# Performance work log

Hardware: AMD Instinct MI355X
Metric: run time of the kernel (lower is better)

## Reference

```python
import jax, jax.numpy as jnp
import numpy as np

NEG_SLOPE = 0.2

def gat_layer(x, src, dst, W, a_src, a_dst, bias, heads, out_ch, concat):
    N = x.shape[0]
    h = (x @ W).reshape(N, heads, out_ch)                      # [N,H,C]
    alpha_s = jnp.sum(h * a_src, axis=-1)                      # [N,H]
    alpha_d = jnp.sum(h * a_dst, axis=-1)                      # [N,H]
    e = jax.nn.leaky_relu(alpha_s[src] + alpha_d[dst], NEG_SLOPE)  # [E,H]
    m = jax.ops.segment_max(e, dst, num_segments=N)            # segment softmax over incoming edges
    e = jnp.exp(e - m[dst])
    denom = jax.ops.segment_sum(e, dst, num_segments=N)
    alpha = e / denom[dst]                                     # [E,H]
    out = jax.ops.segment_sum(alpha[:, :, None] * h[src], dst, num_segments=N)  # [N,H,C]
    out = out.reshape(N, heads * out_ch) if concat else out.mean(axis=1)
    return out + bias

def _glorot(key, shape, fan):
    return jax.random.normal(key, shape, dtype=jnp.float32) * (1.0 / np.sqrt(fan))

def setup_inputs() -> dict:
    key = jax.random.key(0)
    ks = jax.random.split(key, 16)
    N, E, F_IN, H = 50000, 1600000, 128, 2
    x = jax.random.normal(ks[0], (N, F_IN), dtype=jnp.float32)
    edge_index = jax.random.randint(ks[1], (2, E), 0, N, dtype=jnp.int32)
    w1  = _glorot(ks[2], (F_IN, H * 32), F_IN)
    as1 = _glorot(ks[3], (H, 32), 32); ad1 = _glorot(ks[4], (H, 32), 32)
    b1  = jnp.zeros((H * 32,), jnp.float32)
    w2  = _glorot(ks[5], (H * 32, H * 64), H * 32)
    as2 = _glorot(ks[6], (H, 64), 64); ad2 = _glorot(ks[7], (H, 64), 64)
    b2  = jnp.zeros((H * 64,), jnp.float32)
    # layer 3: 128 -> 64, heads=1, concat=False
    w3  = _glorot(ks[8], (H * 64, 64), H * 64)
    as3 = _glorot(ks[9], (1, 64), 64); ad3 = _glorot(ks[10], (1, 64), 64)
    b3  = jnp.zeros((64,), jnp.float32)
    fcw = _glorot(ks[11], (64, 512), 64)
    fcb = jnp.zeros((512,), jnp.float32)
    return dict(x=x, edge_index=edge_index, w1=w1, as1=as1, ad1=ad1, b1=b1,
                w2=w2, as2=as2, ad2=ad2, b2=b2, w3=w3, as3=as3, ad3=ad3, b3=b3,
                fcw=fcw, fcb=fcb)

def reference(x, edge_index, w1, as1, ad1, b1, w2, as2, ad2, b2, w3, as3, ad3, b3, fcw, fcb):
    N = x.shape[0]
    # PyG GATConv default: add self-loops
    loops = jnp.arange(N, dtype=edge_index.dtype)
    src = jnp.concatenate([edge_index[0], loops])
    dst = jnp.concatenate([edge_index[1], loops])
    h = jax.nn.relu(gat_layer(x, src, dst, w1, as1, ad1, b1, heads=2, out_ch=32, concat=True))
    h = jax.nn.relu(gat_layer(h, src, dst, w2, as2, ad2, b2, heads=2, out_ch=64, concat=True))
    h = jax.nn.relu(gat_layer(h, src, dst, w3, as3, ad3, b3, heads=1, out_ch=64, concat=False))
    return jax.nn.relu(h @ fcw + fcb)
```

## Files before the change

kernel.cpp:

```cpp
#include <hip/hip_runtime.h>
#include <hip/hip_fp16.h>
#include <math.h>


typedef _Float16 h2_t __attribute__((ext_vector_type(2)));
typedef _Float16 f16x8 __attribute__((ext_vector_type(8)));
typedef float f32x4 __attribute__((ext_vector_type(4)));

__device__ __forceinline__ h2_t as_h2(unsigned int u) {
    union { unsigned int u; h2_t h; } x; x.u = u; return x.h;
}

__device__ __forceinline__ float fdot2(h2_t a, h2_t b, float c) {
#if __has_builtin(__builtin_amdgcn_fdot2)
    return __builtin_amdgcn_fdot2(a, b, c, false);
#else
    return c + (float)a[0] * (float)b[0] + (float)a[1] * (float)b[1];
#endif
}

__global__ void cvt_kernel(
        const float* __restrict__ x, __half* __restrict__ xh, int n4,
        const float* __restrict__ w1, const float* __restrict__ w2,
        const float* __restrict__ w3, const float* __restrict__ fcw,
        __half* __restrict__ o1, __half* __restrict__ o2,
        __half* __restrict__ o3, __half* __restrict__ o4T,
        int XB) {
    const int b = blockIdx.x;
    if (b < XB) {
        int i = b * 256 + threadIdx.x;
        if (i < n4) {
            float4 v = ((const float4*)x)[i];
            __half2 a, c;
            a.x = (__half)v.x; a.y = (__half)v.y;
            c.x = (__half)v.z; c.y = (__half)v.w;
            ((__half2*)xh)[2 * i]     = a;
            ((__half2*)xh)[2 * i + 1] = c;
        }
    } else {
        int i = (b - XB) * 256 + threadIdx.x;
        if (i < 8192)       o1[i]         = (__half)w1[i];
        else if (i < 16384) o2[i - 8192]  = (__half)w2[i - 8192];
        else if (i < 24576) o3[i - 16384] = (__half)w3[i - 16384];
        else if (i < 57344) {
            int j = i - 24576;
            int k = j >> 9, c = j & 511;
            o4T[c * 64 + k] = (__half)fcw[j];
        }
    }
}

#define SCAN_NB 256

__global__ __launch_bounds__(256) void scanA_kernel(const int* __restrict__ cnt,
                                                    int N, int* __restrict__ bsum) {
    __shared__ int red[256];
    const int chunk = (N + SCAN_NB - 1) / SCAN_NB;
    const int lo = blockIdx.x * chunk;
    const int len = min(N - lo, chunk);
    int s = 0;
    for (int i = threadIdx.x; i < len; i += 256) s += cnt[lo + i];
    red[threadIdx.x] = s;
    __syncthreads();
    for (int off = 128; off >= 1; off >>= 1) {
        if (threadIdx.x < off) red[threadIdx.x] += red[threadIdx.x + off];
        __syncthreads();
    }
    if (threadIdx.x == 0) bsum[blockIdx.x] = red[0];
}

__global__ __launch_bounds__(256) void scanB_kernel(int* __restrict__ bsum,
                                                    int* __restrict__ bbase) {
    __shared__ int s[256];
    int v = bsum[threadIdx.x];
    s[threadIdx.x] = v;
    __syncthreads();
    for (int off = 1; off < 256; off <<= 1) {
        int t = (threadIdx.x >= off) ? s[threadIdx.x - off] : 0;
        __syncthreads();
        s[threadIdx.x] += t;
        __syncthreads();
    }
    bbase[threadIdx.x] = s[threadIdx.x] - v;
}

__global__ __launch_bounds__(256) void scanC_kernel(const int* __restrict__ cnt,
                                                    int N, int Etot,
                                                    const int* __restrict__ bbase,
                                                    int* __restrict__ row_ptr) {
    __shared__ int s[256];
    const int chunk = (N + SCAN_NB - 1) / SCAN_NB;
    const int lo = blockIdx.x * chunk;
    const int len = min(N - lo, chunk);
    const int t = threadIdx.x;
    int v = (t < len) ? cnt[lo + t] : 0;
    s[t] = v;
    __syncthreads();
    for (int off = 1; off < 256; off <<= 1) {
        int u = (t >= off) ? s[t - off] : 0;
        __syncthreads();
        s[t] += u;
        __syncthreads();
    }
    if (t < len) row_ptr[lo + t] = bbase[blockIdx.x] + s[t] - v;
    if (blockIdx.x == 0 && t == 0) row_ptr[N] = Etot;
}

__global__ void scatter_kernel(const int* __restrict__ ei, int E, int N,
                               const int* __restrict__ row_ptr,
                               const int* __restrict__ rank,
                               int* __restrict__ csr_src) {
    const int Etot = E + N;
    const int T = gridDim.x * blockDim.x;
    int e = blockIdx.x * blockDim.x + threadIdx.x;
#pragma unroll 4
    for (int u = 0; u < 4; ++u, e += T) {
        if (e < Etot) {
            int src, dst;
            if (e < E) { src = ei[e]; dst = ei[E + e]; }
            else       { src = e - E; dst = e - E; }
            csr_src[row_ptr[dst] + rank[e]] = src;
        }
    }
}

template <int K, int CHUNK, int RB, int ALPHA, bool COUNT>
__global__ __launch_bounds__(256) void gemm16_kernel(
        const __half* __restrict__ in,
        const __half* __restrict__ Wh,
        __half* __restrict__ out,
        const float* __restrict__ a_src,
        const float* __restrict__ a_dst,
        float* __restrict__ alpS,
        float* __restrict__ alpD,
        int N, int M,
        const int* __restrict__ ei, int E,
        int* __restrict__ cnt, int* __restrict__ rank,
        int GGEMM) {
    constexpr int PL = CHUNK / 64;
    constexpr int K4 = K / 4;
    __shared__ uint2 wlds[K4 * CHUNK];

    if (COUNT && blockIdx.x >= GGEMM) {
        const int Etot = E + N;
        const int T = (gridDim.x - GGEMM) * 256;
        int e = (blockIdx.x - GGEMM) * 256 + threadIdx.x;
#pragma unroll 7
        for (int u = 0; u < 7; ++u, e += T) {
            if (e < Etot) {
                int dst = (e < E) ? ei[E + e] : (e - E);
                rank[e] = atomicAdd(&cnt[dst], 1);
            }
        }
        return;
    }
    const int GSTRIDE = COUNT ? GGEMM : gridDim.x;

    const unsigned short* wsrc = (const unsigned short*)Wh;
    for (int idx = threadIdx.x; idx < K4 * CHUNK; idx += 256) {
        int k4 = idx / CHUNK, c = idx % CHUNK;
        const unsigned short* wp = wsrc + (size_t)(4 * k4) * M + c;
        uint2 v;
        v.x = (unsigned int)wp[0]     | ((unsigned int)wp[M] << 16);
        v.y = (unsigned int)wp[2 * M] | ((unsigned int)wp[3 * M] << 16);
        wlds[idx] = v;
    }
    __syncthreads();

    const int wid  = threadIdx.x >> 6;
    const int lane = threadIdx.x & 63;

    float aSv[PL], aDv[PL];
#pragma unroll
    for (int j = 0; j < PL; ++j) {
        aSv[j] = a_src[lane + 64 * j];
        aDv[j] = a_dst[lane + 64 * j];
    }

    const int groups = (N + RB - 1) / RB;
    for (int g = blockIdx.x * 4 + wid; g < groups; g += GSTRIDE * 4) {
        const int n0 = g * RB;
        const bool full = (n0 + RB <= N);

        float acc[RB][PL];
#pragma unroll
        for (int r = 0; r < RB; ++r)
#pragma unroll
            for (int j = 0; j < PL; ++j) acc[r][j] = 0.0f;

        const uint2* xp = (const uint2*)(in + (size_t)n0 * K);

        if (full) {
            uint2 xv[RB], xn[RB];
#pragma unroll
            for (int r = 0; r < RB; ++r) xv[r] = xp[r * K4];
#pragma unroll 2
            for (int k4 = 0; k4 < K4; ++k4) {
                if (k4 + 1 < K4) {
#pragma unroll
                    for (int r = 0; r < RB; ++r)
                        xn[r] = xp[r * K4 + k4 + 1];
                }
#pragma unroll
                for (int j = 0; j < PL; ++j) {
                    uint2 wv = wlds[k4 * CHUNK + lane + 64 * j];
#pragma unroll
                    for (int r = 0; r < RB; ++r) {
                        acc[r][j] = fdot2(as_h2(xv[r].x), as_h2(wv.x), acc[r][j]);
                        acc[r][j] = fdot2(as_h2(xv[r].y), as_h2(wv.y), acc[r][j]);
                    }
                }
                if (k4 + 1 < K4) {
#pragma unroll
                    for (int r = 0; r < RB; ++r) xv[r] = xn[r];
                }
            }
        } else {
#pragma unroll 1
            for (int k4 = 0; k4 < K4; ++k4) {
#pragma unroll 1
                for (int r = 0; r < RB; ++r) {
                    if (n0 + r >= N) break;
                    uint2 xr = xp[(size_t)r * K4 + k4];
#pragma unroll
                    for (int j = 0; j < PL; ++j) {
                        uint2 wv = wlds[k4 * CHUNK + lane + 64 * j];
                        acc[r][j] = fdot2(as_h2(xr.x), as_h2(wv.x), acc[r][j]);
                        acc[r][j] = fdot2(as_h2(xr.y), as_h2(wv.y), acc[r][j]);
                    }
                }
            }
        }

#pragma unroll
        for (int r = 0; r < RB; ++r) {
            if (!full && n0 + r >= N) break;
            const int n = n0 + r;
#pragma unroll
            for (int j = 0; j < PL; ++j)
                out[(size_t)n * M + lane + 64 * j] = (__half)acc[r][j];

            float ps[PL], pd[PL];
#pragma unroll
            for (int j = 0; j < PL; ++j) { ps[j] = acc[r][j] * aSv[j]; pd[j] = acc[r][j] * aDv[j]; }
            const int m0 = (ALPHA == 1) ? 16 : 32;
            for (int mm = m0; mm >= 1; mm >>= 1) {
#pragma unroll
                for (int j = 0; j < PL; ++j) {
                    ps[j] += __shfl_xor(ps[j], mm, 64);
                    pd[j] += __shfl_xor(pd[j], mm, 64);
                }
            }
            if (ALPHA == 1) {
                if ((lane & 31) == 0) {
                    int idx = n * 2 + (lane >> 5);
                    alpS[idx] = ps[0]; alpD[idx] = pd[0];
                }
            } else if (ALPHA == 2) {
                if (lane == 0) {
#pragma unroll
                    for (int j = 0; j < PL; ++j) {
                        alpS[n * 2 + j] = ps[j]; alpD[n * 2 + j] = pd[j];
                    }
                }
            } else {
                if (lane == 0) { alpS[n] = ps[0]; alpD[n] = pd[0]; }
            }
        }
    }
}

__global__ __launch_bounds__(256) void fcmfma_kernel(
        const __half* __restrict__ in,
        const __half* __restrict__ WT,
        const float* __restrict__ bias,
        float* __restrict__ out,
        int N, int NT) {
    const int wid  = threadIdx.x >> 6;
    const int lane = threadIdx.x & 63;
    const int cb = blockIdx.y * 256 + wid * 64;
    const int r  = lane & 15;
    const int kg = lane >> 4;

    f16x8 bfrag[4][2];
#pragma unroll
    for (int t = 0; t < 4; ++t)
#pragma unroll
        for (int kf = 0; kf < 2; ++kf)
            bfrag[t][kf] = *(const f16x8*)(WT + (size_t)(cb + t * 16 + r) * 64 + kf * 32 + kg * 8);
    float bs[4];
#pragma unroll
    for (int t = 0; t < 4; ++t) bs[t] = bias[cb + t * 16 + r];

    const int rt0 = blockIdx.x * 5;
#pragma unroll 1
    for (int q = 0; q < 5; ++q) {
        const int rt = rt0 + q;
        if (rt >= NT) break;
        const int n0 = rt * 16;
        f16x8 a0 = *(const f16x8*)(in + (size_t)(n0 + r) * 64 + kg * 8);
        f16x8 a1 = *(const f16x8*)(in + (size_t)(n0 + r) * 64 + 32 + kg * 8);
#pragma unroll
        for (int t = 0; t < 4; ++t) {
            f32x4 acc = {0.0f, 0.0f, 0.0f, 0.0f};
            acc = __builtin_amdgcn_mfma_f32_16x16x32_f16(a0, bfrag[t][0], acc, 0, 0, 0);
            acc = __builtin_amdgcn_mfma_f32_16x16x32_f16(a1, bfrag[t][1], acc, 0, 0, 0);
#pragma unroll
            for (int i = 0; i < 4; ++i) {
                int grow = n0 + kg * 4 + i;
                if (grow < N)
                    out[(size_t)grow * 512 + cb + t * 16 + r] = fmaxf(acc[i] + bs[t], 0.0f);
            }
        }
    }
}

template <int H, int C>
__global__ __launch_bounds__(256) void aggregate_kernel(
        const __half* __restrict__ h,
        const float* __restrict__ alpha_s,
        const float* __restrict__ alpha_d,
        const int* __restrict__ row_ptr,
        const int* __restrict__ csr_src,
        const float* __restrict__ bias,
        __half* __restrict__ out, int N) {
    constexpr int M = H * C;
    __shared__ int   ss[4][64];
    __shared__ float sp[4][128];
    const int wid  = threadIdx.x >> 6;
    const int lane = threadIdx.x & 63;
    const int n = blockIdx.x * 4 + wid;
    if (n >= N) return;

    const int lo = row_ptr[n], hi = row_ptr[n + 1];
    const int myhead = (H == 2) ? (lane / C) : 0;

    float adv[H];
#pragma unroll
    for (int t = 0; t < H; ++t) adv[t] = alpha_d[n * H + t];

    float m[H], den[H], acc = 0.0f;
#pragma unroll
    for (int t = 0; t < H; ++t) { m[t] = -INFINITY; den[t] = 0.0f; }

    for (int e0 = lo; e0 < hi; e0 += 64) {
        const int idx = e0 + lane;
        const bool valid = idx < hi;
        const int src_l = csr_src[valid ? idx : hi - 1];

        float lg[H];
        if (H == 2) {
            float2 as = ((const float2*)alpha_s)[src_l];
            lg[0] = as.x + adv[0];
            lg[1] = as.y + adv[1];
        } else {
            lg[0] = alpha_s[src_l] + adv[0];
        }
#pragma unroll
        for (int t = 0; t < H; ++t) {
            float v = lg[t];
            v = v > 0.0f ? v : 0.2f * v;
            lg[t] = valid ? v : -INFINITY;
        }
        float cm[H];
#pragma unroll
        for (int t = 0; t < H; ++t) cm[t] = lg[t];
        for (int mm = 32; mm >= 1; mm >>= 1) {
#pragma unroll
            for (int t = 0; t < H; ++t)
                cm[t] = fmaxf(cm[t], __shfl_xor(cm[t], mm, 64));
        }
        float sc[H];
#pragma unroll
        for (int t = 0; t < H; ++t) {
            float mnew = fmaxf(m[t], cm[t]);
            sc[t] = __expf(m[t] - mnew);
            den[t] *= sc[t];
            m[t] = mnew;
        }
        acc *= (H == 1) ? sc[0] : (myhead == 0 ? sc[0] : sc[1]);

        float p[H], dsum[H];
#pragma unroll
        for (int t = 0; t < H; ++t) { p[t] = __expf(lg[t] - m[t]); dsum[t] = p[t]; }
        for (int mm = 32; mm >= 1; mm >>= 1) {
#pragma unroll
            for (int t = 0; t < H; ++t)
                dsum[t] += __shfl_xor(dsum[t], mm, 64);
        }
#pragma unroll
        for (int t = 0; t < H; ++t) den[t] += dsum[t];

        ss[wid][lane] = src_l;
        if (H == 2) ((float2*)sp[wid])[lane] = make_float2(p[0], p[1]);
        else        sp[wid][lane] = p[0];

        int nu = hi - e0; if (nu > 64) nu = 64;
        int u = 0;
#pragma unroll 1
        for (; u + 8 <= nu; u += 8) {
            int su[8];
#pragma unroll
            for (int t = 0; t < 8; ++t)
                su[t] = __builtin_amdgcn_readfirstlane(ss[wid][u + t]);
            float hv[8];
#pragma unroll
            for (int t = 0; t < 8; ++t)
                hv[t] = __half2float(h[(size_t)su[t] * M + lane]);
            if (H == 2) {
                const float2* pb = (const float2*)sp[wid];
#pragma unroll
                for (int t = 0; t < 8; ++t) {
                    float2 q = pb[u + t];
                    acc += (myhead == 0 ? q.x : q.y) * hv[t];
                }
            } else {
#pragma unroll
                for (int t = 0; t < 8; ++t)
                    acc += sp[wid][u + t] * hv[t];
            }
        }
#pragma unroll 1
        for (; u < nu; ++u) {
            int su = __builtin_amdgcn_readfirstlane(ss[wid][u]);
            float hv = __half2float(h[(size_t)su * M + lane]);
            if (H == 2) {
                float2 q = ((const float2*)sp[wid])[u];
                acc += (myhead == 0 ? q.x : q.y) * hv;
            } else {
                acc += sp[wid][u] * hv;
            }
        }
    }

    float dv = (H == 1) ? den[0] : (myhead == 0 ? den[0] : den[1]);
    float v = acc / dv + bias[lane];
    out[(size_t)n * M + lane] = (__half)fmaxf(v, 0.0f);
}

__global__ __launch_bounds__(256) void aggregate2_kernel(
        const __half* __restrict__ h,
        const float* __restrict__ alpha_s,
        const float* __restrict__ alpha_d,
        const int* __restrict__ row_ptr,
        const int* __restrict__ csr_src,
        const float* __restrict__ bias,
        __half* __restrict__ out, int N) {
    __shared__ int   ss[4][64];
    __shared__ float sp[4][64];
    const int wid  = threadIdx.x >> 6;
    const int lane = threadIdx.x & 63;
    const int gw   = blockIdx.x * 4 + wid;
    const int n    = gw >> 1;
    const int hd   = gw & 1;
    if (n >= N) return;

    const int lo = row_ptr[n], hi = row_ptr[n + 1];
    const float adv = alpha_d[n * 2 + hd];

    float m = -INFINITY, den = 0.0f, acc = 0.0f;

    for (int e0 = lo; e0 < hi; e0 += 64) {
        const int idx = e0 + lane;
        const bool valid = idx < hi;
        const int src_l = csr_src[valid ? idx : hi - 1];

        float lg = alpha_s[src_l * 2 + hd] + adv;
        lg = lg > 0.0f ? lg : 0.2f * lg;
        if (!valid) lg = -INFINITY;

        float cm = lg;
        for (int mm = 32; mm >= 1; mm >>= 1)
            cm = fmaxf(cm, __shfl_xor(cm, mm, 64));

        float mnew = fmaxf(m, cm);
        float sc = __expf(m - mnew);
        den *= sc; acc *= sc; m = mnew;

        float p = __expf(lg - m), ds = p;
        for (int mm = 32; mm >= 1; mm >>= 1)
            ds += __shfl_xor(ds, mm, 64);
        den += ds;

        ss[wid][lane] = src_l;
        sp[wid][lane] = p;

        int nu = hi - e0; if (nu > 64) nu = 64;
        int u = 0;
#pragma unroll 1
        for (; u + 8 <= nu; u += 8) {
            int su[8];
#pragma unroll
            for (int t = 0; t < 8; ++t)
                su[t] = __builtin_amdgcn_readfirstlane(ss[wid][u + t]);
            float hv[8];
#pragma unroll
            for (int t = 0; t < 8; ++t)
                hv[t] = __half2float(h[(size_t)su[t] * 128 + hd * 64 + lane]);
#pragma unroll
            for (int t = 0; t < 8; ++t)
                acc += sp[wid][u + t] * hv[t];
        }
#pragma unroll 1
        for (; u < nu; ++u) {
            int su = __builtin_amdgcn_readfirstlane(ss[wid][u]);
            acc += sp[wid][u] * __half2float(h[(size_t)su * 128 + hd * 64 + lane]);
        }
    }

    float v = acc / den + bias[hd * 64 + lane];
    out[(size_t)n * 128 + hd * 64 + lane] = (__half)fmaxf(v, 0.0f);
}


extern "C" void kernel_launch(void* const* d_in, const int* in_sizes, int n_in,
                              void* d_out, int out_size, void* d_ws, size_t ws_size,
                              hipStream_t stream) {
    const float* x   = (const float*)d_in[0];
    const int*   ei  = (const int*)  d_in[1];
    const float* w1  = (const float*)d_in[2];
    const float* as1 = (const float*)d_in[3];
    const float* ad1 = (const float*)d_in[4];
    const float* b1  = (const float*)d_in[5];
    const float* w2  = (const float*)d_in[6];
    const float* as2 = (const float*)d_in[7];
    const float* ad2 = (const float*)d_in[8];
    const float* b2  = (const float*)d_in[9];
    const float* w3  = (const float*)d_in[10];
    const float* as3 = (const float*)d_in[11];
    const float* ad3 = (const float*)d_in[12];
    const float* b3  = (const float*)d_in[13];
    const float* fcw = (const float*)d_in[14];
    const float* fcb = (const float*)d_in[15];
    float* out = (float*)d_out;

    const int N = in_sizes[0] / 128;
    const int E = in_sizes[1] / 2;
    const int Etot = E + N;

    char* p = (char*)d_ws;
    auto alloc = [&](size_t bytes) {
        char* r = p;
        p += (bytes + 255) & ~(size_t)255;
        return r;
    };
    int*    cnt     = (int*)   alloc((size_t)N * 4);
    int*    row_ptr = (int*)   alloc((size_t)(N + 1) * 4);
    int*    rank    = (int*)   alloc((size_t)Etot * 4);
    int*    csr_src = (int*)   alloc((size_t)Etot * 4);
    int*    bsum    = (int*)   alloc((size_t)SCAN_NB * 4);
    int*    bbase   = (int*)   alloc((size_t)SCAN_NB * 4);
    __half* x16     = (__half*)alloc((size_t)N * 128 * 2);
    __half* bufA    = (__half*)alloc((size_t)N * 128 * 2);
    __half* bufB    = (__half*)alloc((size_t)N * 128 * 2);
    __half* bufC    = (__half*)alloc((size_t)(N + 16) * 64 * 2);
    __half* wh1     = (__half*)alloc((size_t)8192 * 2);
    __half* wh2     = (__half*)alloc((size_t)8192 * 2);
    __half* wh3     = (__half*)alloc((size_t)8192 * 2);
    __half* fcwT    = (__half*)alloc((size_t)32768 * 2);
    float*  alpS    = (float*) alloc((size_t)N * 2 * 4);
    float*  alpD    = (float*) alloc((size_t)N * 2 * 4);
    (void)ws_size; (void)n_in; (void)out_size;

    hipMemsetAsync(cnt, 0, (size_t)N * 4, stream);
    const int n4 = N * 32;
    const int XB = (n4 + 255) / 256;
    const int WB = 224;
    cvt_kernel<<<XB + WB, 256, 0, stream>>>(
        x, x16, n4, w1, w2, w3, fcw, wh1, wh2, wh3, fcwT, XB);

    int gb  = (N + 3) / 4;
    int gb2 = (2 * N + 3) / 4;
    const int GB16 = 2048;
    const int GG1  = 1024;
    const int GC1  = 1024;

    gemm16_kernel<128, 64, 8, 1, true><<<dim3(GG1 + GC1, 1), 256, 0, stream>>>(
        x16, wh1, bufA, as1, ad1, alpS, alpD, N, 64, ei, E, cnt, rank, GG1);

    scanA_kernel<<<SCAN_NB, 256, 0, stream>>>(cnt, N, bsum);
    scanB_kernel<<<1, 256, 0, stream>>>(bsum, bbase);
    scanC_kernel<<<SCAN_NB, 256, 0, stream>>>(cnt, N, Etot, bbase, row_ptr);
    const int CB = (Etot / 4 + 255) / 256 + 1;
    scatter_kernel<<<CB, 256, 0, stream>>>(ei, E, N, row_ptr, rank, csr_src);

    aggregate_kernel<2, 32><<<gb, 256, 0, stream>>>(bufA, alpS, alpD, row_ptr, csr_src, b1, bufB, N);

    gemm16_kernel<64, 128, 8, 2, false><<<dim3(GB16, 1), 256, 0, stream>>>(
        bufB, wh2, bufA, as2, ad2, alpS, alpD, N, 128, nullptr, 0, nullptr, nullptr, GB16);
    aggregate2_kernel<<<gb2, 256, 0, stream>>>(bufA, alpS, alpD, row_ptr, csr_src, b2, bufB, N);

    gemm16_kernel<128, 64, 8, 3, false><<<dim3(GB16, 1), 256, 0, stream>>>(
        bufB, wh3, bufA, as3, ad3, alpS, alpD, N, 64, nullptr, 0, nullptr, nullptr, GB16);
    aggregate_kernel<1, 64><<<gb, 256, 0, stream>>>(bufA, alpS, alpD, row_ptr, csr_src, b3, bufC, N);

    const int NT = (N + 15) / 16;
    const int GX = (NT + 4) / 5;
    fcmfma_kernel<<<dim3(GX, 2), 256, 0, stream>>>(
        bufC, fcwT, fcb, out, N, NT);
}
```

Before: 587.8 us.

## Replace layer-2 and layer-3 fdot2 GEMMs with MFMA kernels using transposed weights

Layers 2 and 3 now do their dense transforms with new MFMA kernels (16x16x32 f16) instead of the generic fdot2-based kernel. The weights are stored transposed in the conversion kernel so B fragments load contiguously, and the attention logits are reduced across the 16-lane groups of the MFMA output. Layer 1 keeps the fdot2 path with edge counting, now specialised into its own kernel. The aim is to move GEMM work to the matrix cores, at the cost of padded buffers and fragment loads that read past N into the padding rows.

```diff
diff --git a/kernel.cpp b/kernel.cpp
--- a/kernel.cpp
+++ b/kernel.cpp
@@ -23,8 +23,8 @@
         const float* __restrict__ x, __half* __restrict__ xh, int n4,
         const float* __restrict__ w1, const float* __restrict__ w2,
         const float* __restrict__ w3, const float* __restrict__ fcw,
-        __half* __restrict__ o1, __half* __restrict__ o2,
-        __half* __restrict__ o3, __half* __restrict__ o4T,
+        __half* __restrict__ o1, __half* __restrict__ o2T,
+        __half* __restrict__ o3T, __half* __restrict__ o4T,
         int XB) {
     const int b = blockIdx.x;
     if (b < XB) {
@@ -39,10 +39,17 @@
         }
     } else {
         int i = (b - XB) * 256 + threadIdx.x;
-        if (i < 8192)       o1[i]         = (__half)w1[i];
-        else if (i < 16384) o2[i - 8192]  = (__half)w2[i - 8192];
-        else if (i < 24576) o3[i - 16384] = (__half)w3[i - 16384];
-        else if (i < 57344) {
+        if (i < 8192) {
+            o1[i] = (__half)w1[i];
+        } else if (i < 16384) {
+            int j = i - 8192;
+            int k = j >> 7, c = j & 127;
+            o2T[c * 64 + k] = (__half)w2[j];
+        } else if (i < 24576) {
+            int j = i - 16384;
+            int k = j >> 6, c = j & 63;
+            o3T[c * 128 + k] = (__half)w3[j];
+        } else if (i < 57344) {
             int j = i - 24576;
             int k = j >> 9, c = j & 511;
             o4T[c * 64 + k] = (__half)fcw[j];
@@ -124,8 +131,7 @@
     }
 }
 
-template <int K, int CHUNK, int RB, int ALPHA, bool COUNT>
-__global__ __launch_bounds__(256) void gemm16_kernel(
+__global__ __launch_bounds__(256) void gemm1_count_kernel(
         const __half* __restrict__ in,
         const __half* __restrict__ Wh,
         __half* __restrict__ out,
@@ -133,15 +139,14 @@
         const float* __restrict__ a_dst,
         float* __restrict__ alpS,
         float* __restrict__ alpD,
-        int N, int M,
+        int N,
         const int* __restrict__ ei, int E,
         int* __restrict__ cnt, int* __restrict__ rank,
         int GGEMM) {
-    constexpr int PL = CHUNK / 64;
-    constexpr int K4 = K / 4;
+    constexpr int K4 = 32, CHUNK = 64, M = 64, RB = 8;
     __shared__ uint2 wlds[K4 * CHUNK];
 
-    if (COUNT && blockIdx.x >= GGEMM) {
+    if (blockIdx.x >= GGEMM) {
         const int Etot = E + N;
         const int T = (gridDim.x - GGEMM) * 256;
         int e = (blockIdx.x - GGEMM) * 256 + threadIdx.x;
@@ -154,7 +159,6 @@
         }
         return;
     }
-    const int GSTRIDE = COUNT ? GGEMM : gridDim.x;
 
     const unsigned short* wsrc = (const unsigned short*)Wh;
     for (int idx = threadIdx.x; idx < K4 * CHUNK; idx += 256) {
@@ -169,26 +173,19 @@
 
     const int wid  = threadIdx.x >> 6;
     const int lane = threadIdx.x & 63;
-
-    float aSv[PL], aDv[PL];
-#pragma unroll
-    for (int j = 0; j < PL; ++j) {
-        aSv[j] = a_src[lane + 64 * j];
-        aDv[j] = a_dst[lane + 64 * j];
-    }
+    const float aSv = a_src[lane];
+    const float aDv = a_dst[lane];
 
     const int groups = (N + RB - 1) / RB;
-    for (int g = blockIdx.x * 4 + wid; g < groups; g += GSTRIDE * 4) {
+    for (int g = blockIdx.x * 4 + wid; g < groups; g += GGEMM * 4) {
         const int n0 = g * RB;
         const bool full = (n0 + RB <= N);
 
-        float acc[RB][PL];
-#pragma unroll
-        for (int r = 0; r < RB; ++r)
-#pragma unroll
-            for (int j = 0; j < PL; ++j) acc[r][j] = 0.0f;
-
-        const uint2* xp = (const uint2*)(in + (size_t)n0 * K);
+        float acc[RB];
+#pragma unroll
+        for (int r = 0; r < RB; ++r) acc[r] = 0.0f;
+
+        const uint2* xp = (const uint2*)(in + (size_t)n0 * 128);
 
         if (full) {
             uint2 xv[RB], xn[RB];
@@ -201,14 +198,11 @@
                     for (int r = 0; r < RB; ++r)
                         xn[r] = xp[r * K4 + k4 + 1];
                 }
-#pragma unroll
-                for (int j = 0; j < PL; ++j) {
-                    uint2 wv = wlds[k4 * CHUNK + lane + 64 * j];
-#pragma unroll
-                    for (int r = 0; r < RB; ++r) {
-                        acc[r][j] = fdot2(as_h2(xv[r].x), as_h2(wv.x), acc[r][j]);
-                        acc[r][j] = fdot2(as_h2(xv[r].y), as_h2(wv.y), acc[r][j]);
-                    }
+                uint2 wv = wlds[k4 * CHUNK + lane];
+#pragma unroll
+                for (int r = 0; r < RB; ++r) {
+                    acc[r] = fdot2(as_h2(xv[r].x), as_h2(wv.x), acc[r]);
+                    acc[r] = fdot2(as_h2(xv[r].y), as_h2(wv.y), acc[r]);
                 }
                 if (k4 + 1 < K4) {
 #pragma unroll
@@ -218,16 +212,13 @@
         } else {
 #pragma unroll 1
             for (int k4 = 0; k4 < K4; ++k4) {
+                uint2 wv = wlds[k4 * CHUNK + lane];
 #pragma unroll 1
                 for (int r = 0; r < RB; ++r) {
                     if (n0 + r >= N) break;
                     uint2 xr = xp[(size_t)r * K4 + k4];
-#pragma unroll
-                    for (int j = 0; j < PL; ++j) {
-                        uint2 wv = wlds[k4 * CHUNK + lane + 64 * j];
-                        acc[r][j] = fdot2(as_h2(xr.x), as_h2(wv.x), acc[r][j]);
-                        acc[r][j] = fdot2(as_h2(xr.y), as_h2(wv.y), acc[r][j]);
-                    }
+                    acc[r] = fdot2(as_h2(xr.x), as_h2(wv.x), acc[r]);
+                    acc[r] = fdot2(as_h2(xr.y), as_h2(wv.y), acc[r]);
                 }
             }
         }
@@ -236,36 +227,172 @@
         for (int r = 0; r < RB; ++r) {
             if (!full && n0 + r >= N) break;
             const int n = n0 + r;
-#pragma unroll
-            for (int j = 0; j < PL; ++j)
-                out[(size_t)n * M + lane + 64 * j] = (__half)acc[r][j];
-
-            float ps[PL], pd[PL];
-#pragma unroll
-            for (int j = 0; j < PL; ++j) { ps[j] = acc[r][j] * aSv[j]; pd[j] = acc[r][j] * aDv[j]; }
-            const int m0 = (ALPHA == 1) ? 16 : 32;
-            for (int mm = m0; mm >= 1; mm >>= 1) {
-#pragma unroll
-                for (int j = 0; j < PL; ++j) {
-                    ps[j] += __shfl_xor(ps[j], mm, 64);
-                    pd[j] += __shfl_xor(pd[j], mm, 64);
-                }
-            }
-            if (ALPHA == 1) {
-                if ((lane & 31) == 0) {
-                    int idx = n * 2 + (lane >> 5);
-                    alpS[idx] = ps[0]; alpD[idx] = pd[0];
-                }
-            } else if (ALPHA == 2) {
-                if (lane == 0) {
-#pragma unroll
-                    for (int j = 0; j < PL; ++j) {
-                        alpS[n * 2 + j] = ps[j]; alpD[n * 2 + j] = pd[j];
-                    }
-                }
-            } else {
-                if (lane == 0) { alpS[n] = ps[0]; alpD[n] = pd[0]; }
-            }
+            out[(size_t)n * M + lane] = (__half)acc[r];
+
+            float ps = acc[r] * aSv, pd = acc[r] * aDv;
+            for (int mm = 16; mm >= 1; mm >>= 1) {
+                ps += __shfl_xor(ps, mm, 64);
+                pd += __shfl_xor(pd, mm, 64);
+            }
+            if ((lane & 31) == 0) {
+                int idx = n * 2 + (lane >> 5);
+                alpS[idx] = ps; alpD[idx] = pd;
+            }
+        }
+    }
+}
+
+__global__ __launch_bounds__(256) void gemm2_mfma_kernel(
+        const __half* __restrict__ in,
+        const __half* __restrict__ WT,
+        __half* __restrict__ out,
+        const float* __restrict__ a_src,
+        const float* __restrict__ a_dst,
+        float* __restrict__ alpS,
+        float* __restrict__ alpD,
+        int N, int NT) {
+    const int wid     = threadIdx.x >> 6;
+    const int lane    = threadIdx.x & 63;
+    const int rowgrp  = wid >> 1;
+    const int colhalf = wid & 1;
+    const int cb = colhalf * 64;
+    const int r  = lane & 15;
+    const int kg = lane >> 4;
+
+    f16x8 bfrag[4][2];
+#pragma unroll
+    for (int t = 0; t < 4; ++t)
+#pragma unroll
+        for (int kf = 0; kf < 2; ++kf)
+            bfrag[t][kf] = *(const f16x8*)(WT + (size_t)(cb + t * 16 + r) * 64 + kf * 32 + kg * 8);
+    float asv[4], adv[4];
+#pragma unroll
+    for (int t = 0; t < 4; ++t) {
+        asv[t] = a_src[cb + t * 16 + r];
+        adv[t] = a_dst[cb + t * 16 + r];
+    }
+
+    const int rt = blockIdx.x * 2 + rowgrp;
+    if (rt >= NT) return;
+    const int n0 = rt * 16;
+
+    f16x8 a0 = *(const f16x8*)(in + (size_t)(n0 + r) * 64 + kg * 8);
+    f16x8 a1 = *(const f16x8*)(in + (size_t)(n0 + r) * 64 + 32 + kg * 8);
+
+    f32x4 acc[4];
+#pragma unroll
+    for (int t = 0; t < 4; ++t) {
+        acc[t] = (f32x4){0.0f, 0.0f, 0.0f, 0.0f};
+        acc[t] = __builtin_amdgcn_mfma_f32_16x16x32_f16(a0, bfrag[t][0], acc[t], 0, 0, 0);
+        acc[t] = __builtin_amdgcn_mfma_f32_16x16x32_f16(a1, bfrag[t][1], acc[t], 0, 0, 0);
+    }
+
+#pragma unroll
+    for (int i = 0; i < 4; ++i) {
+        int grow = n0 + kg * 4 + i;
+        if (grow < N) {
+#pragma unroll
+            for (int t = 0; t < 4; ++t)
+                out[(size_t)grow * 128 + cb + t * 16 + r] = (__half)acc[t][i];
+        }
+    }
+    float ps[4], pd[4];
+#pragma unroll
+    for (int i = 0; i < 4; ++i) {
+        ps[i] = acc[0][i] * asv[0] + acc[1][i] * asv[1] + acc[2][i] * asv[2] + acc[3][i] * asv[3];
+        pd[i] = acc[0][i] * adv[0] + acc[1][i] * adv[1] + acc[2][i] * adv[2] + acc[3][i] * adv[3];
+    }
+    for (int mm = 8; mm >= 1; mm >>= 1) {
+#pragma unroll
+        for (int i = 0; i < 4; ++i) {
+            ps[i] += __shfl_xor(ps[i], mm, 64);
+            pd[i] += __shfl_xor(pd[i], mm, 64);
+        }
+    }
+    if (r == 0) {
+#pragma unroll
+        for (int i = 0; i < 4; ++i) {
+            int n = n0 + kg * 4 + i;
+            if (n < N) {
+                alpS[n * 2 + colhalf] = ps[i];
+                alpD[n * 2 + colhalf] = pd[i];
+            }
+        }
+    }
+}
+
+__global__ __launch_bounds__(256) void gemm3_mfma_kernel(
+        const __half* __restrict__ in,
+        const __half* __restrict__ WT,
+        __half* __restrict__ out,
+        const float* __restrict__ a_src,
+        const float* __restrict__ a_dst,
+        float* __restrict__ alpS,
+        float* __restrict__ alpD,
+        int N, int NT) {
+    const int wid  = threadIdx.x >> 6;
+    const int lane = threadIdx.x & 63;
+    const int r  = lane & 15;
+    const int kg = lane >> 4;
+
+    f16x8 bfrag[4][4];
+#pragma unroll
+    for (int t = 0; t < 4; ++t)
+#pragma unroll
+        for (int kf = 0; kf < 4; ++kf)
+            bfrag[t][kf] = *(const f16x8*)(WT + (size_t)(t * 16 + r) * 128 + kf * 32 + kg * 8);
+    float asv[4], adv[4];
+#pragma unroll
+    for (int t = 0; t < 4; ++t) {
+        asv[t] = a_src[t * 16 + r];
+        adv[t] = a_dst[t * 16 + r];
+    }
+
+    const int rt = blockIdx.x * 4 + wid;
+    if (rt >= NT) return;
+    const int n0 = rt * 16;
+
+    f16x8 a[4];
+#pragma unroll
+    for (int kf = 0; kf < 4; ++kf)
+        a[kf] = *(const f16x8*)(in + (size_t)(n0 + r) * 128 + kf * 32 + kg * 8);
+
+    f32x4 acc[4];
+#pragma unroll
+    for (int t = 0; t < 4; ++t) {
+        acc[t] = (f32x4){0.0f, 0.0f, 0.0f, 0.0f};
+#pragma unroll
+        for (int kf = 0; kf < 4; ++kf)
+            acc[t] = __builtin_amdgcn_mfma_f32_16x16x32_f16(a[kf], bfrag[t][kf], acc[t], 0, 0, 0);
+    }
+
+#pragma unroll
+    for (int i = 0; i < 4; ++i) {
+        int grow = n0 + kg * 4 + i;
+        if (grow < N) {
+#pragma unroll
+            for (int t = 0; t < 4; ++t)
+                out[(size_t)grow * 64 + t * 16 + r] = (__half)acc[t][i];
+        }
+    }
+    float ps[4], pd[4];
+#pragma unroll
+    for (int i = 0; i < 4; ++i) {
+        ps[i] = acc[0][i] * asv[0] + acc[1][i] * asv[1] + acc[2][i] * asv[2] + acc[3][i] * asv[3];
+        pd[i] = acc[0][i] * adv[0] + acc[1][i] * adv[1] + acc[2][i] * adv[2] + acc[3][i] * adv[3];
+    }
+    for (int mm = 8; mm >= 1; mm >>= 1) {
+#pragma unroll
+        for (int i = 0; i < 4; ++i) {
+            ps[i] += __shfl_xor(ps[i], mm, 64);
+            pd[i] += __shfl_xor(pd[i], mm, 64);
+        }
+    }
+    if (r == 0) {
+#pragma unroll
+        for (int i = 0; i < 4; ++i) {
+            int n = n0 + kg * 4 + i;
+            if (n < N) { alpS[n] = ps[i]; alpD[n] = pd[i]; }
         }
     }
 }
@@ -551,12 +678,12 @@
     int*    bsum    = (int*)   alloc((size_t)SCAN_NB * 4);
     int*    bbase   = (int*)   alloc((size_t)SCAN_NB * 4);
     __half* x16     = (__half*)alloc((size_t)N * 128 * 2);
-    __half* bufA    = (__half*)alloc((size_t)N * 128 * 2);
-    __half* bufB    = (__half*)alloc((size_t)N * 128 * 2);
+    __half* bufA    = (__half*)alloc((size_t)(N + 16) * 128 * 2);
+    __half* bufB    = (__half*)alloc((size_t)(N + 16) * 128 * 2);
     __half* bufC    = (__half*)alloc((size_t)(N + 16) * 64 * 2);
     __half* wh1     = (__half*)alloc((size_t)8192 * 2);
-    __half* wh2     = (__half*)alloc((size_t)8192 * 2);
-    __half* wh3     = (__half*)alloc((size_t)8192 * 2);
+    __half* wh2T    = (__half*)alloc((size_t)8192 * 2);
+    __half* wh3T    = (__half*)alloc((size_t)8192 * 2);
     __half* fcwT    = (__half*)alloc((size_t)32768 * 2);
     float*  alpS    = (float*) alloc((size_t)N * 2 * 4);
     float*  alpD    = (float*) alloc((size_t)N * 2 * 4);
@@ -567,16 +694,16 @@
     const int XB = (n4 + 255) / 256;
     const int WB = 224;
     cvt_kernel<<<XB + WB, 256, 0, stream>>>(
-        x, x16, n4, w1, w2, w3, fcw, wh1, wh2, wh3, fcwT, XB);
+        x, x16, n4, w1, w2, w3, fcw, wh1, wh2T, wh3T, fcwT, XB);
 
     int gb  = (N + 3) / 4;
     int gb2 = (2 * N + 3) / 4;
-    const int GB16 = 2048;
-    const int GG1  = 1024;
-    const int GC1  = 1024;
-
-    gemm16_kernel<128, 64, 8, 1, true><<<dim3(GG1 + GC1, 1), 256, 0, stream>>>(
-        x16, wh1, bufA, as1, ad1, alpS, alpD, N, 64, ei, E, cnt, rank, GG1);
+    const int GG1 = 1024;
+    const int GC1 = 1024;
+    const int NT  = (N + 15) / 16;
+
+    gemm1_count_kernel<<<dim3(GG1 + GC1, 1), 256, 0, stream>>>(
+        x16, wh1, bufA, as1, ad1, alpS, alpD, N, ei, E, cnt, rank, GG1);
 
     scanA_kernel<<<SCAN_NB, 256, 0, stream>>>(cnt, N, bsum);
     scanB_kernel<<<1, 256, 0, stream>>>(bsum, bbase);
@@ -586,15 +713,14 @@
 
     aggregate_kernel<2, 32><<<gb, 256, 0, stream>>>(bufA, alpS, alpD, row_ptr, csr_src, b1, bufB, N);
 
-    gemm16_kernel<64, 128, 8, 2, false><<<dim3(GB16, 1), 256, 0, stream>>>(
-        bufB, wh2, bufA, as2, ad2, alpS, alpD, N, 128, nullptr, 0, nullptr, nullptr, GB16);
+    gemm2_mfma_kernel<<<(NT + 1) / 2, 256, 0, stream>>>(
+        bufB, wh2T, bufA, as2, ad2, alpS, alpD, N, NT);
     aggregate2_kernel<<<gb2, 256, 0, stream>>>(bufA, alpS, alpD, row_ptr, csr_src, b2, bufB, N);
 
-    gemm16_kernel<128, 64, 8, 3, false><<<dim3(GB16, 1), 256, 0, stream>>>(
-        bufB, wh3, bufA, as3, ad3, alpS, alpD, N, 64, nullptr, 0, nullptr, nullptr, GB16);
+    gemm3_mfma_kernel<<<(NT + 3) / 4, 256, 0, stream>>>(
+        bufB, wh3T, bufA, as3, ad3, alpS, alpD, N, NT);
     aggregate_kernel<1, 64><<<gb, 256, 0, stream>>>(bufA, alpS, alpD, row_ptr, csr_src, b3, bufC, N);
 
-    const int NT = (N + 15) / 16;
     const int GX = (NT + 4) / 5;
     fcmfma_kernel<<<dim3(GX, 2), 256, 0, stream>>>(
         bufC, fcwT, fcb, out, N, NT);
```

Result: faster. 517.8 us, median of 2 (-11.9%).
